# Optimization experiments

Measured on AMD Instinct MI355X. Metric: run time of the kernel, lower is better.

## Reference

```python
import jax, jax.numpy as jnp
import numpy as np

D_MODEL = 1024
N_HEADS = 16
D_HEAD = D_MODEL // N_HEADS
B = 4
S = 1024


def setup_inputs() -> dict:
    key = jax.random.key(0)
    ks = jax.random.split(key, 7)
    scale = 0.02
    return {
        "x": jax.random.normal(ks[0], (B, S, D_MODEL), dtype=jnp.float32),
        "relative_pos_embeddings": jax.random.normal(ks[1], (S, S, D_HEAD), dtype=jnp.float32),
        "Wq": jax.random.normal(ks[2], (D_MODEL, D_MODEL), dtype=jnp.float32) * scale,
        "Wk": jax.random.normal(ks[3], (D_HEAD, D_MODEL), dtype=jnp.float32) * scale,
        "Wv": jax.random.normal(ks[4], (D_HEAD, D_MODEL), dtype=jnp.float32) * scale,
        "Wo": jax.random.normal(ks[5], (D_MODEL, D_MODEL), dtype=jnp.float32) * scale,
        "bo": jax.random.normal(ks[6], (D_MODEL,), dtype=jnp.float32) * scale,
    }


def reference(x, relative_pos_embeddings, Wq, Wk, Wv, Wo, bo):
    b, s, d_model = x.shape
    h, dh = N_HEADS, D_HEAD
    scale = 1.0 / np.sqrt(dh).astype(np.float32)
    # projections (torch Linear: y = x @ W^T)
    q = (x @ Wq.T).reshape(b, s, h, dh).transpose(0, 2, 1, 3)  # [b,h,s,dh]
    k = x @ Wk.T  # [b,s,dh] single shared KV head (MQA)
    v = x @ Wv.T  # [b,s,dh]
    # content-to-content scores
    c2c = jnp.einsum('bhid,bjd->bhij', q, k)
    # content-to-position: c2p[b,h,i,j] = q[b,h,i,:] . rel[i,j,:]
    c2p = jnp.einsum('bhid,ijd->bhij', q, relative_pos_embeddings)
    attn = jax.nn.softmax((c2c + c2p) * scale, axis=-1)
    context = jnp.einsum('bhij,bjd->bhid', attn, v)  # [b,h,s,dh]
    context = context.transpose(0, 2, 1, 3).reshape(b, s, h * dh)
    return context @ Wo.T + bo
```

## Files before the change

### kernel.cpp

```cpp
#include <hip/hip_runtime.h>
#include <hip/hip_bf16.h>

#define S_LEN 1024
#define DM 1024
#define NH 16
#define DH 64
#define BB 4

typedef short s16x8 __attribute__((ext_vector_type(8)));
typedef short s16x4 __attribute__((ext_vector_type(4)));
typedef float f32x4 __attribute__((ext_vector_type(4)));

__device__ __forceinline__ unsigned short f2b(float f) {
    __hip_bfloat16 h = __float2bfloat16(f);
    return __builtin_bit_cast(unsigned short, h);
}

__global__ void convert_all(const float* __restrict__ x, const float* __restrict__ wq,
                            const float* __restrict__ wk, const float* __restrict__ wv,
                            const float* __restrict__ wo,
                            unsigned short* __restrict__ xb, unsigned short* __restrict__ wqb,
                            unsigned short* __restrict__ wkb, unsigned short* __restrict__ wvb,
                            unsigned short* __restrict__ wob) {
    const int tid = blockIdx.x * blockDim.x + threadIdx.x;
    const int stride = gridDim.x * blockDim.x;
    auto conv = [&](const float* src, unsigned short* dst, int n4) {
        const float4* s4 = (const float4*)src;
        s16x4* d4 = (s16x4*)dst;
        for (int i = tid; i < n4; i += stride) {
            float4 f = s4[i];
            s16x4 o = { (short)f2b(f.x), (short)f2b(f.y), (short)f2b(f.z), (short)f2b(f.w) };
            d4[i] = o;
        }
    };
    conv(x,  xb,  (BB * S_LEN * DM) / 4);
    conv(wq, wqb, (DM * DM) / 4);
    conv(wk, wkb, (DH * DM) / 4);
    conv(wv, wvb, (DH * DM) / 4);
    conv(wo, wob, (DM * DM) / 4);
}

template <int MODE>
__global__ __launch_bounds__(256) void gemm_bt(
    const unsigned short* __restrict__ A, const unsigned short* __restrict__ Bw,
    int M, int N, int K,
    unsigned short* __restrict__ outb,
    unsigned short* __restrict__ koutb, unsigned short* __restrict__ vtout,
    float* __restrict__ outf, const float* __restrict__ bias) {
    __shared__ unsigned short As[128 * 72];
    __shared__ unsigned short Bs[128 * 72];
    const int t = threadIdx.x;
    const int w = t >> 6, lane = t & 63, qd = lane >> 4, c = lane & 15;
    const int m0 = blockIdx.x * 128, n0 = blockIdx.y * 128;
    const int wm = (w >> 1) * 64, wn = (w & 1) * 64;

    f32x4 acc[4][4];
    for (int mb = 0; mb < 4; ++mb)
        for (int nb = 0; nb < 4; ++nb) acc[mb][nb] = (f32x4){0.f, 0.f, 0.f, 0.f};

    for (int kk = 0; kk < K; kk += 64) {
        __syncthreads();
#pragma unroll
        for (int it = 0; it < 4; ++it) {
            int vi = it * 256 + t;
            int row = vi >> 3, col8 = (vi & 7) * 8;
            *(s16x8*)&As[row * 72 + col8] = *(const s16x8*)&A[(size_t)(m0 + row) * K + kk + col8];
            *(s16x8*)&Bs[row * 72 + col8] = *(const s16x8*)&Bw[(size_t)(n0 + row) * K + kk + col8];
        }
        __syncthreads();
#pragma unroll
        for (int kb = 0; kb < 2; ++kb) {
            s16x8 af[4], bf[4];
#pragma unroll
            for (int mb = 0; mb < 4; ++mb)
                af[mb] = *(const s16x8*)&As[(wm + mb * 16 + c) * 72 + kb * 32 + qd * 8];
#pragma unroll
            for (int nb = 0; nb < 4; ++nb)
                bf[nb] = *(const s16x8*)&Bs[(wn + nb * 16 + c) * 72 + kb * 32 + qd * 8];
#pragma unroll
            for (int mb = 0; mb < 4; ++mb)
#pragma unroll
                for (int nb = 0; nb < 4; ++nb)
                    acc[mb][nb] = __builtin_amdgcn_mfma_f32_16x16x32_bf16(af[mb], bf[nb], acc[mb][nb], 0, 0, 0);
        }
    }

#pragma unroll
    for (int mb = 0; mb < 4; ++mb)
#pragma unroll
        for (int nb = 0; nb < 4; ++nb)
#pragma unroll
            for (int r = 0; r < 4; ++r) {
                int row = m0 + wm + mb * 16 + qd * 4 + r;
                int col = n0 + wn + nb * 16 + c;
                float v = acc[mb][nb][r];
                if (MODE == 0) {
                    outb[(size_t)row * N + col] = f2b(v);
                } else if (MODE == 2) {
                    outf[(size_t)row * N + col] = v + bias[col];
                } else {
                    if (col < 64)
                        koutb[(size_t)row * 64 + col] = f2b(v);
                    else
                        vtout[(size_t)(row >> 10) * 65536 + (size_t)(col - 64) * 1024 + (row & 1023)] = f2b(v);
                }
            }
}

__global__ __launch_bounds__(256) void attn_kernel(
    const unsigned short* __restrict__ qb, const unsigned short* __restrict__ kg,
    const unsigned short* __restrict__ vt, const float* __restrict__ rel,
    unsigned short* __restrict__ ctx) {
    __shared__ unsigned short rel_s[128 * 72];
    __shared__ unsigned short P_s[4 * 16 * 136];
    const int i = blockIdx.x;
    const int t = threadIdx.x;
    const int w = t >> 6, lane = t & 63, qd = lane >> 4, c = lane & 15;
    const int b = w;

    s16x8 aq[2];
    {
        const size_t qbase = ((size_t)(b * S_LEN + i)) * DM + (size_t)c * DH + qd * 8;
        aq[0] = *(const s16x8*)&qb[qbase];
        aq[1] = *(const s16x8*)&qb[qbase + 32];
    }

    f32x4 oacc[4];
    for (int nb = 0; nb < 4; ++nb) oacc[nb] = (f32x4){0.f, 0.f, 0.f, 0.f};
    float m_run[4], l_run[4];
    for (int r = 0; r < 4; ++r) { m_run[r] = -INFINITY; l_run[r] = 0.f; }

    const float C2 = 0.125f * 1.44269504088896f;

    for (int jt = 0; jt < 8; ++jt) {
        const int j0 = jt * 128;
        __syncthreads();
        {
            const size_t base = ((size_t)i * S_LEN + j0) * DH;
#pragma unroll
            for (int it = 0; it < 8; ++it) {
                int vi = it * 256 + t;
                int row = vi >> 4, d4 = (vi & 15) * 4;
                float4 f = *(const float4*)&rel[base + (size_t)row * 64 + d4];
                s16x4 o = { (short)f2b(f.x), (short)f2b(f.y), (short)f2b(f.z), (short)f2b(f.w) };
                *(s16x4*)&rel_s[row * 72 + d4] = o;
            }
        }
        __syncthreads();

        f32x4 sa[8];
#pragma unroll
        for (int jb = 0; jb < 8; ++jb) sa[jb] = (f32x4){0.f, 0.f, 0.f, 0.f};
#pragma unroll
        for (int kb = 0; kb < 2; ++kb) {
#pragma unroll
            for (int jb = 0; jb < 8; ++jb) {
                s16x8 rf = *(const s16x8*)&rel_s[(jb * 16 + c) * 72 + kb * 32 + qd * 8];
                sa[jb] = __builtin_amdgcn_mfma_f32_16x16x32_bf16(aq[kb], rf, sa[jb], 0, 0, 0);
                s16x8 kf = *(const s16x8*)&kg[((size_t)b * S_LEN + j0 + jb * 16 + c) * DH + kb * 32 + qd * 8];
                sa[jb] = __builtin_amdgcn_mfma_f32_16x16x32_bf16(aq[kb], kf, sa[jb], 0, 0, 0);
            }
        }

        float alpha[4];
#pragma unroll
        for (int r = 0; r < 4; ++r) {
            float mx = -INFINITY;
#pragma unroll
            for (int jb = 0; jb < 8; ++jb) {
                sa[jb][r] *= C2;
                mx = fmaxf(mx, sa[jb][r]);
            }
            mx = fmaxf(mx, __shfl_xor(mx, 1));
            mx = fmaxf(mx, __shfl_xor(mx, 2));
            mx = fmaxf(mx, __shfl_xor(mx, 4));
            mx = fmaxf(mx, __shfl_xor(mx, 8));
            float mnew = fmaxf(m_run[r], mx);
            alpha[r] = exp2f(m_run[r] - mnew);
            m_run[r] = mnew;
            float s = 0.f;
#pragma unroll
            for (int jb = 0; jb < 8; ++jb) {
                float p = exp2f(sa[jb][r] - mnew);
                s += p;
                P_s[(w * 16 + qd * 4 + r) * 136 + jb * 16 + c] = f2b(p);
            }
            s += __shfl_xor(s, 1);
            s += __shfl_xor(s, 2);
            s += __shfl_xor(s, 4);
            s += __shfl_xor(s, 8);
            l_run[r] = l_run[r] * alpha[r] + s;
        }
#pragma unroll
        for (int nb = 0; nb < 4; ++nb)
#pragma unroll
            for (int r = 0; r < 4; ++r) oacc[nb][r] *= alpha[r];

        __syncthreads();

#pragma unroll
        for (int kk2 = 0; kk2 < 4; ++kk2) {
            s16x8 pf = *(const s16x8*)&P_s[(w * 16 + c) * 136 + kk2 * 32 + qd * 8];
#pragma unroll
            for (int nb = 0; nb < 4; ++nb) {
                s16x8 vf = *(const s16x8*)&vt[(size_t)b * 65536 + (size_t)(nb * 16 + c) * 1024 + j0 + kk2 * 32 + qd * 8];
                oacc[nb] = __builtin_amdgcn_mfma_f32_16x16x32_bf16(pf, vf, oacc[nb], 0, 0, 0);
            }
        }
    }

#pragma unroll
    for (int nb = 0; nb < 4; ++nb)
#pragma unroll
        for (int r = 0; r < 4; ++r) {
            float o = oacc[nb][r] / l_run[r];
            int h = qd * 4 + r, d = nb * 16 + c;
            ctx[((size_t)b * S_LEN + i) * DM + h * DH + d] = f2b(o);
        }
}

extern "C" void kernel_launch(void* const* d_in, const int* in_sizes, int n_in,
                              void* d_out, int out_size, void* d_ws, size_t ws_size,
                              hipStream_t stream) {
    (void)in_sizes; (void)n_in; (void)out_size; (void)ws_size;
    const float* x   = (const float*)d_in[0];
    const float* rel = (const float*)d_in[1];
    const float* Wq  = (const float*)d_in[2];
    const float* Wk  = (const float*)d_in[3];
    const float* Wv  = (const float*)d_in[4];
    const float* Wo  = (const float*)d_in[5];
    const float* bo  = (const float*)d_in[6];
    float* out = (float*)d_out;

    unsigned short* ws  = (unsigned short*)d_ws;
    unsigned short* xb  = ws;
    unsigned short* wqb = xb + 4194304;
    unsigned short* wkb = wqb + 1048576;
    unsigned short* wvb = wkb + 65536;
    unsigned short* wob = wvb + 65536;
    unsigned short* qbf = wob + 1048576;
    unsigned short* kbf = qbf + 4194304;
    unsigned short* vtb = kbf + 262144;
    unsigned short* ctxb = vtb + 262144;

    convert_all<<<1024, 256, 0, stream>>>(x, Wq, Wk, Wv, Wo, xb, wqb, wkb, wvb, wob);
    gemm_bt<0><<<dim3(32, 8), 256, 0, stream>>>(xb, wqb, 4096, 1024, 1024,
                                                qbf, nullptr, nullptr, nullptr, nullptr);
    gemm_bt<1><<<dim3(32, 1), 256, 0, stream>>>(xb, wkb, 4096, 128, 1024,
                                                nullptr, kbf, vtb, nullptr, nullptr);
    attn_kernel<<<1024, 256, 0, stream>>>(qbf, kbf, vtb, rel, ctxb);
    gemm_bt<2><<<dim3(32, 8), 256, 0, stream>>>(ctxb, wob, 4096, 1024, 1024,
                                                nullptr, nullptr, nullptr, out, bo);
}
```

Measured before the change: 636.5 us.

## Split attention over key chunks with merge kernel, fuse QKV GEMM, use direct LDS loads

Attention is split into four key-range chunks per query row. Each chunk writes partial bf16 outputs plus running max and sum, and a new merge kernel combines them, giving four times more blocks to hide memory latency on the relative-embedding stream. The next relative tile is prefetched into registers while the current one is computed, and K/V loads are hoisted ahead of the MFMAs. The Q and KV projections are fused into a single GEMM launch over 1152 columns, which relies on Wq, Wk and Wv being contiguous in workspace. GEMM tiles shrink to 128x64 and load through global_load_lds without LDS padding. The costs are extra partial-output traffic, an extra launch, and bf16 rounding of the partial results.

```diff
diff --git a/kernel.cpp b/kernel.cpp
--- a/kernel.cpp
+++ b/kernel.cpp
@@ -14,6 +14,15 @@
 __device__ __forceinline__ unsigned short f2b(float f) {
     __hip_bfloat16 h = __float2bfloat16(f);
     return __builtin_bit_cast(unsigned short, h);
+}
+__device__ __forceinline__ float b2f(unsigned short u) {
+    unsigned int v = ((unsigned int)u) << 16;
+    return __builtin_bit_cast(float, v);
+}
+__device__ __forceinline__ void gld16(const unsigned short* g, unsigned short* l) {
+    __builtin_amdgcn_global_load_lds(
+        (const __attribute__((address_space(1))) unsigned int*)g,
+        (__attribute__((address_space(3))) unsigned int*)l, 16, 0, 0);
 }
 
 __global__ void convert_all(const float* __restrict__ x, const float* __restrict__ wq,
@@ -47,38 +56,41 @@
     unsigned short* __restrict__ outb,
     unsigned short* __restrict__ koutb, unsigned short* __restrict__ vtout,
     float* __restrict__ outf, const float* __restrict__ bias) {
-    __shared__ unsigned short As[128 * 72];
-    __shared__ unsigned short Bs[128 * 72];
+    __shared__ unsigned short As[128 * 64];
+    __shared__ unsigned short Bs[64 * 64];
     const int t = threadIdx.x;
     const int w = t >> 6, lane = t & 63, qd = lane >> 4, c = lane & 15;
-    const int m0 = blockIdx.x * 128, n0 = blockIdx.y * 128;
-    const int wm = (w >> 1) * 64, wn = (w & 1) * 64;
-
-    f32x4 acc[4][4];
-    for (int mb = 0; mb < 4; ++mb)
+    const int m0 = blockIdx.x * 128, n0 = blockIdx.y * 64;
+    const int wm = w * 32;
+
+    f32x4 acc[2][4];
+    for (int mb = 0; mb < 2; ++mb)
         for (int nb = 0; nb < 4; ++nb) acc[mb][nb] = (f32x4){0.f, 0.f, 0.f, 0.f};
 
     for (int kk = 0; kk < K; kk += 64) {
         __syncthreads();
 #pragma unroll
-        for (int it = 0; it < 4; ++it) {
-            int vi = it * 256 + t;
-            int row = vi >> 3, col8 = (vi & 7) * 8;
-            *(s16x8*)&As[row * 72 + col8] = *(const s16x8*)&A[(size_t)(m0 + row) * K + kk + col8];
-            *(s16x8*)&Bs[row * 72 + col8] = *(const s16x8*)&Bw[(size_t)(n0 + row) * K + kk + col8];
+        for (int is = 0; is < 4; ++is) {
+            int vi = is * 256 + t;
+            gld16(&A[(size_t)(m0 + (vi >> 3)) * K + kk + (vi & 7) * 8], &As[vi * 8]);
+        }
+#pragma unroll
+        for (int is = 0; is < 2; ++is) {
+            int vi = is * 256 + t;
+            gld16(&Bw[(size_t)(n0 + (vi >> 3)) * K + kk + (vi & 7) * 8], &Bs[vi * 8]);
         }
         __syncthreads();
 #pragma unroll
         for (int kb = 0; kb < 2; ++kb) {
-            s16x8 af[4], bf[4];
-#pragma unroll
-            for (int mb = 0; mb < 4; ++mb)
-                af[mb] = *(const s16x8*)&As[(wm + mb * 16 + c) * 72 + kb * 32 + qd * 8];
+            s16x8 af[2], bf[4];
+#pragma unroll
+            for (int mb = 0; mb < 2; ++mb)
+                af[mb] = *(const s16x8*)&As[(wm + mb * 16 + c) * 64 + kb * 32 + qd * 8];
 #pragma unroll
             for (int nb = 0; nb < 4; ++nb)
-                bf[nb] = *(const s16x8*)&Bs[(wn + nb * 16 + c) * 72 + kb * 32 + qd * 8];
-#pragma unroll
-            for (int mb = 0; mb < 4; ++mb)
+                bf[nb] = *(const s16x8*)&Bs[(nb * 16 + c) * 64 + kb * 32 + qd * 8];
+#pragma unroll
+            for (int mb = 0; mb < 2; ++mb)
 #pragma unroll
                 for (int nb = 0; nb < 4; ++nb)
                     acc[mb][nb] = __builtin_amdgcn_mfma_f32_16x16x32_bf16(af[mb], bf[nb], acc[mb][nb], 0, 0, 0);
@@ -86,34 +98,35 @@
     }
 
 #pragma unroll
-    for (int mb = 0; mb < 4; ++mb)
+    for (int mb = 0; mb < 2; ++mb)
 #pragma unroll
         for (int nb = 0; nb < 4; ++nb)
 #pragma unroll
             for (int r = 0; r < 4; ++r) {
                 int row = m0 + wm + mb * 16 + qd * 4 + r;
-                int col = n0 + wn + nb * 16 + c;
+                int col = n0 + nb * 16 + c;
                 float v = acc[mb][nb][r];
-                if (MODE == 0) {
-                    outb[(size_t)row * N + col] = f2b(v);
-                } else if (MODE == 2) {
-                    outf[(size_t)row * N + col] = v + bias[col];
+                if (MODE == 2) {
+                    outf[(size_t)row * 1024 + col] = v + bias[col];
                 } else {
-                    if (col < 64)
-                        koutb[(size_t)row * 64 + col] = f2b(v);
+                    if (col < 1024)
+                        outb[(size_t)row * 1024 + col] = f2b(v);
+                    else if (col < 1088)
+                        koutb[(size_t)row * 64 + (col - 1024)] = f2b(v);
                     else
-                        vtout[(size_t)(row >> 10) * 65536 + (size_t)(col - 64) * 1024 + (row & 1023)] = f2b(v);
+                        vtout[(size_t)(row >> 10) * 65536 + (size_t)(col - 1088) * 1024 + (row & 1023)] = f2b(v);
                 }
             }
 }
 
-__global__ __launch_bounds__(256) void attn_kernel(
+__global__ __launch_bounds__(256, 3) void attn_kernel(
     const unsigned short* __restrict__ qb, const unsigned short* __restrict__ kg,
     const unsigned short* __restrict__ vt, const float* __restrict__ rel,
-    unsigned short* __restrict__ ctx) {
+    unsigned short* __restrict__ Opart, float* __restrict__ ml) {
     __shared__ unsigned short rel_s[128 * 72];
     __shared__ unsigned short P_s[4 * 16 * 136];
     const int i = blockIdx.x;
+    const int chunk = blockIdx.y;
     const int t = threadIdx.x;
     const int w = t >> 6, lane = t & 63, qd = lane >> 4, c = lane & 15;
     const int b = w;
@@ -132,33 +145,46 @@
 
     const float C2 = 0.125f * 1.44269504088896f;
 
-    for (int jt = 0; jt < 8; ++jt) {
-        const int j0 = jt * 128;
+    const size_t rbase = ((size_t)i * S_LEN + chunk * 256) * DH;
+    float4 pre[8];
+#pragma unroll
+    for (int it = 0; it < 8; ++it)
+        pre[it] = *(const float4*)&rel[rbase + (size_t)(it * 256 + t) * 4];
+
+#pragma unroll
+    for (int jt = 0; jt < 2; ++jt) {
+        const int j0 = chunk * 256 + jt * 128;
         __syncthreads();
-        {
-            const size_t base = ((size_t)i * S_LEN + j0) * DH;
-#pragma unroll
-            for (int it = 0; it < 8; ++it) {
-                int vi = it * 256 + t;
-                int row = vi >> 4, d4 = (vi & 15) * 4;
-                float4 f = *(const float4*)&rel[base + (size_t)row * 64 + d4];
-                s16x4 o = { (short)f2b(f.x), (short)f2b(f.y), (short)f2b(f.z), (short)f2b(f.w) };
-                *(s16x4*)&rel_s[row * 72 + d4] = o;
-            }
+#pragma unroll
+        for (int it = 0; it < 8; ++it) {
+            int vi = it * 256 + t;
+            float4 f = pre[it];
+            s16x4 o = { (short)f2b(f.x), (short)f2b(f.y), (short)f2b(f.z), (short)f2b(f.w) };
+            *(s16x4*)&rel_s[(vi >> 4) * 72 + (vi & 15) * 4] = o;
         }
         __syncthreads();
+        if (jt == 0) {
+#pragma unroll
+            for (int it = 0; it < 8; ++it)
+                pre[it] = *(const float4*)&rel[rbase + 128 * 64 + (size_t)(it * 256 + t) * 4];
+        }
 
         f32x4 sa[8];
 #pragma unroll
         for (int jb = 0; jb < 8; ++jb) sa[jb] = (f32x4){0.f, 0.f, 0.f, 0.f};
 #pragma unroll
         for (int kb = 0; kb < 2; ++kb) {
+            s16x8 kf[8], rf[8];
+#pragma unroll
+            for (int jb = 0; jb < 8; ++jb)
+                kf[jb] = *(const s16x8*)&kg[((size_t)b * S_LEN + j0 + jb * 16 + c) * DH + kb * 32 + qd * 8];
+#pragma unroll
+            for (int jb = 0; jb < 8; ++jb)
+                rf[jb] = *(const s16x8*)&rel_s[(jb * 16 + c) * 72 + kb * 32 + qd * 8];
 #pragma unroll
             for (int jb = 0; jb < 8; ++jb) {
-                s16x8 rf = *(const s16x8*)&rel_s[(jb * 16 + c) * 72 + kb * 32 + qd * 8];
-                sa[jb] = __builtin_amdgcn_mfma_f32_16x16x32_bf16(aq[kb], rf, sa[jb], 0, 0, 0);
-                s16x8 kf = *(const s16x8*)&kg[((size_t)b * S_LEN + j0 + jb * 16 + c) * DH + kb * 32 + qd * 8];
-                sa[jb] = __builtin_amdgcn_mfma_f32_16x16x32_bf16(aq[kb], kf, sa[jb], 0, 0, 0);
+                sa[jb] = __builtin_amdgcn_mfma_f32_16x16x32_bf16(aq[kb], rf[jb], sa[jb], 0, 0, 0);
+                sa[jb] = __builtin_amdgcn_mfma_f32_16x16x32_bf16(aq[kb], kf[jb], sa[jb], 0, 0, 0);
             }
         }
 
@@ -196,27 +222,67 @@
 #pragma unroll
             for (int r = 0; r < 4; ++r) oacc[nb][r] *= alpha[r];
 
-        __syncthreads();
-
 #pragma unroll
         for (int kk2 = 0; kk2 < 4; ++kk2) {
+            s16x8 vf[4];
+#pragma unroll
+            for (int nb = 0; nb < 4; ++nb)
+                vf[nb] = *(const s16x8*)&vt[(size_t)b * 65536 + (size_t)(nb * 16 + c) * 1024 + j0 + kk2 * 32 + qd * 8];
             s16x8 pf = *(const s16x8*)&P_s[(w * 16 + c) * 136 + kk2 * 32 + qd * 8];
 #pragma unroll
-            for (int nb = 0; nb < 4; ++nb) {
-                s16x8 vf = *(const s16x8*)&vt[(size_t)b * 65536 + (size_t)(nb * 16 + c) * 1024 + j0 + kk2 * 32 + qd * 8];
-                oacc[nb] = __builtin_amdgcn_mfma_f32_16x16x32_bf16(pf, vf, oacc[nb], 0, 0, 0);
-            }
+            for (int nb = 0; nb < 4; ++nb)
+                oacc[nb] = __builtin_amdgcn_mfma_f32_16x16x32_bf16(pf, vf[nb], oacc[nb], 0, 0, 0);
         }
     }
 
 #pragma unroll
     for (int nb = 0; nb < 4; ++nb)
 #pragma unroll
+        for (int r = 0; r < 4; ++r)
+            Opart[((size_t)chunk * S_LEN + i) * 4096 + b * 1024 + (qd * 4 + r) * 64 + nb * 16 + c] =
+                f2b(oacc[nb][r]);
+    if (c == 0) {
+#pragma unroll
         for (int r = 0; r < 4; ++r) {
-            float o = oacc[nb][r] / l_run[r];
-            int h = qd * 4 + r, d = nb * 16 + c;
-            ctx[((size_t)b * S_LEN + i) * DM + h * DH + d] = f2b(o);
-        }
+            size_t base = (((size_t)chunk * S_LEN + i) * 64 + b * 16 + qd * 4 + r) * 2;
+            ml[base] = m_run[r];
+            ml[base + 1] = l_run[r];
+        }
+    }
+}
+
+__global__ __launch_bounds__(256) void merge_kernel(
+    const unsigned short* __restrict__ Opart, const float* __restrict__ ml,
+    unsigned short* __restrict__ ctx) {
+    const int i = blockIdx.x, t = threadIdx.x;
+#pragma unroll
+    for (int k = 0; k < 4; ++k) {
+        int e = k * 1024 + t * 4;
+        int bh = e >> 6;
+        float m_c[4], l_c[4];
+#pragma unroll
+        for (int cc = 0; cc < 4; ++cc) {
+            size_t base = (((size_t)cc * S_LEN + i) * 64 + bh) * 2;
+            m_c[cc] = ml[base];
+            l_c[cc] = ml[base + 1];
+        }
+        float mstar = fmaxf(fmaxf(m_c[0], m_c[1]), fmaxf(m_c[2], m_c[3]));
+        float o0 = 0.f, o1 = 0.f, o2 = 0.f, o3 = 0.f, lsum = 0.f;
+#pragma unroll
+        for (int cc = 0; cc < 4; ++cc) {
+            float wgt = exp2f(m_c[cc] - mstar);
+            lsum += l_c[cc] * wgt;
+            s16x4 ov = *(const s16x4*)&Opart[((size_t)cc * S_LEN + i) * 4096 + e];
+            o0 += b2f((unsigned short)ov[0]) * wgt;
+            o1 += b2f((unsigned short)ov[1]) * wgt;
+            o2 += b2f((unsigned short)ov[2]) * wgt;
+            o3 += b2f((unsigned short)ov[3]) * wgt;
+        }
+        float inv = 1.0f / lsum;
+        s16x4 o = { (short)f2b(o0 * inv), (short)f2b(o1 * inv),
+                    (short)f2b(o2 * inv), (short)f2b(o3 * inv) };
+        *(s16x4*)&ctx[((size_t)(e >> 10) * S_LEN + i) * 1024 + (e & 1023)] = o;
+    }
 }
 
 extern "C" void kernel_launch(void* const* d_in, const int* in_sizes, int n_in,
@@ -233,22 +299,23 @@
     float* out = (float*)d_out;
 
     unsigned short* ws  = (unsigned short*)d_ws;
-    unsigned short* xb  = ws;
-    unsigned short* wqb = xb + 4194304;
-    unsigned short* wkb = wqb + 1048576;
-    unsigned short* wvb = wkb + 65536;
-    unsigned short* wob = wvb + 65536;
-    unsigned short* qbf = wob + 1048576;
-    unsigned short* kbf = qbf + 4194304;
-    unsigned short* vtb = kbf + 262144;
+    unsigned short* xb   = ws;
+    unsigned short* wqb  = xb + 4194304;
+    unsigned short* wkb  = wqb + 1048576;
+    unsigned short* wvb  = wkb + 65536;
+    unsigned short* wob  = wvb + 65536;
+    unsigned short* qbf  = wob + 1048576;
+    unsigned short* kbf  = qbf + 4194304;
+    unsigned short* vtb  = kbf + 262144;
     unsigned short* ctxb = vtb + 262144;
+    unsigned short* Opart = ctxb + 4194304;
+    float* mlf = (float*)(Opart + 16777216);
 
     convert_all<<<1024, 256, 0, stream>>>(x, Wq, Wk, Wv, Wo, xb, wqb, wkb, wvb, wob);
-    gemm_bt<0><<<dim3(32, 8), 256, 0, stream>>>(xb, wqb, 4096, 1024, 1024,
-                                                qbf, nullptr, nullptr, nullptr, nullptr);
-    gemm_bt<1><<<dim3(32, 1), 256, 0, stream>>>(xb, wkb, 4096, 128, 1024,
-                                                nullptr, kbf, vtb, nullptr, nullptr);
-    attn_kernel<<<1024, 256, 0, stream>>>(qbf, kbf, vtb, rel, ctxb);
-    gemm_bt<2><<<dim3(32, 8), 256, 0, stream>>>(ctxb, wob, 4096, 1024, 1024,
-                                                nullptr, nullptr, nullptr, out, bo);
-}
+    gemm_bt<0><<<dim3(32, 18), 256, 0, stream>>>(xb, wqb, 4096, 1152, 1024,
+                                                 qbf, kbf, vtb, nullptr, nullptr);
+    attn_kernel<<<dim3(1024, 4), 256, 0, stream>>>(qbf, kbf, vtb, rel, Opart, mlf);
+    merge_kernel<<<1024, 256, 0, stream>>>(Opart, mlf, ctxb);
+    gemm_bt<2><<<dim3(32, 16), 256, 0, stream>>>(ctxb, wob, 4096, 1024, 1024,
+                                                 nullptr, nullptr, nullptr, out, bo);
+}
```

Result: faster. 534.4 us (-16.0%).
